# Kernel optimization log

Measured on AMD Instinct MI355X. Metric: run time of the kernel, lower is better.

Reference implementation:

```python
import jax, jax.numpy as jnp
import numpy as np

SEQ, B, N, F_IN = 128, 32, 1024, 16
NHID, G_FEAT, H = 2, 4, 256


def setup_inputs() -> dict:
    key = jax.random.key(0)
    ks = jax.random.split(key, 14)
    inp = {}
    inp['x'] = jax.random.normal(ks[0], (SEQ, B, N, F_IN), jnp.float32)
    # row-scaled random dense adjacency (keeps activations well-conditioned)
    inp['adj'] = jax.random.uniform(ks[1], (N, N), jnp.float32) * (1.0 / N)
    inp['gc1_w'] = jax.random.normal(ks[2], (F_IN, NHID), jnp.float32) * 0.3
    inp['gc1_b'] = jax.random.normal(ks[3], (NHID,), jnp.float32) * 0.1
    inp['gc2_w'] = jax.random.normal(ks[4], (NHID, G_FEAT), jnp.float32) * 0.3
    inp['gc2_b'] = jax.random.normal(ks[5], (G_FEAT,), jnp.float32) * 0.1
    in0 = G_FEAT * N  # GRU layer-0 input size = G_feat * num_nodes
    inp['w_ih_l0'] = jax.random.normal(ks[6], (3 * H, in0), jnp.float32) * 0.02
    inp['w_hh_l0'] = jax.random.normal(ks[7], (3 * H, H), jnp.float32) * 0.05
    inp['b_ih_l0'] = jax.random.normal(ks[8], (3 * H,), jnp.float32) * 0.05
    inp['b_hh_l0'] = jax.random.normal(ks[9], (3 * H,), jnp.float32) * 0.05
    inp['w_ih_l1'] = jax.random.normal(ks[10], (3 * H, H), jnp.float32) * 0.05
    inp['w_hh_l1'] = jax.random.normal(ks[11], (3 * H, H), jnp.float32) * 0.05
    inp['b_ih_l1'] = jax.random.normal(ks[12], (3 * H,), jnp.float32) * 0.05
    inp['b_hh_l1'] = jax.random.normal(ks[13], (3 * H,), jnp.float32) * 0.05
    return inp


def gru_layer(x_seq, h0, w_ih, w_hh, b_ih, b_hh):
    # torch nn.GRU gate math, gate order (r, z, n)
    def step(h, x_t):
        gi = x_t @ w_ih.T + b_ih          # (B, 3H)
        gh = h @ w_hh.T + b_hh            # (B, 3H)
        i_r, i_z, i_n = jnp.split(gi, 3, axis=-1)
        h_r, h_z, h_n = jnp.split(gh, 3, axis=-1)
        r = jax.nn.sigmoid(i_r + h_r)
        z = jax.nn.sigmoid(i_z + h_z)
        n = jnp.tanh(i_n + r * h_n)
        h_new = (1.0 - z) * n + z * h
        return h_new, h_new
    hT, out = jax.lax.scan(step, h0, x_seq)
    return out, hT


def reference(x, adj, gc1_w, gc1_b, gc2_w, gc2_b,
              w_ih_l0, w_hh_l0, b_ih_l0, b_hh_l0,
              w_ih_l1, w_hh_l1, b_ih_l1, b_hh_l1):
    # GCN, vectorized over (seq, batch). GraphConvolution: adj @ (x @ W) + b
    s = jnp.einsum('sbnf,fh->sbnh', x, gc1_w) + gc1_b
    s = jnp.einsum('mn,sbnh->sbmh', adj, s)
    s = jax.nn.relu(s)
    # dropout inactive in eval mode
    s = jnp.einsum('sbnh,hg->sbng', s, gc2_w) + gc2_b
    s = jnp.einsum('mn,sbng->sbmg', adj, s)
    s = jax.nn.log_softmax(s, axis=2)  # dim=1 of per-step (B, N, G) == node axis
    out = s.reshape(SEQ, B, N * G_FEAT)  # .view(batch, -1) per step, stacked
    h0 = jnp.zeros((B, H), out.dtype)
    out, h1 = gru_layer(out, h0, w_ih_l0, w_hh_l0, b_ih_l0, b_hh_l0)
    out, h2 = gru_layer(out, h0, w_ih_l1, w_hh_l1, b_ih_l1, b_hh_l1)
    hn = jnp.stack([h1, h2])  # (n_layers, B, H)
    return out, hn
```

## Files before the change

kernel.cpp:

```cpp
#include <hip/hip_runtime.h>
#include <stdint.h>

constexpr int SEQL = 128;
constexpr int BAT  = 32;
constexpr int NN   = 1024;
constexpr int FIN  = 16;
constexpr int HH   = 256;
constexpr int PQ   = SEQL * BAT;
constexpr float LSM_SHIFT = 6.9314718055994531f;

using f32x4 = __attribute__((ext_vector_type(4))) float;
using s16x8 = __attribute__((ext_vector_type(8))) short;

__device__ __forceinline__ unsigned short f2bf(float x) {
  unsigned u = __float_as_uint(x);
  u += 0x7fffu + ((u >> 16) & 1u);
  return (unsigned short)(u >> 16);
}
__device__ __forceinline__ float sigm(float x) { return 1.f / (1.f + __expf(-x)); }

__device__ __forceinline__ void gl_lds16(const void* g, void* l) {
  __builtin_amdgcn_global_load_lds(
      (const __attribute__((address_space(1))) void*)g,
      (__attribute__((address_space(3))) void*)l, 16, 0, 0);
}

#if __has_builtin(__builtin_amdgcn_fdot2_f32_bf16)
typedef __bf16 bf16x2_t __attribute__((ext_vector_type(2)));
__device__ __forceinline__ float dot2bf(unsigned w, unsigned h, float acc) {
  return __builtin_amdgcn_fdot2_f32_bf16(__builtin_bit_cast(bf16x2_t, w),
                                         __builtin_bit_cast(bf16x2_t, h), acc, false);
}
#else
__device__ __forceinline__ float dot2bf(unsigned w, unsigned h, float acc) {
  acc += __uint_as_float(w << 16) * __uint_as_float(h << 16);
  acc += __uint_as_float(w & 0xffff0000u) * __uint_as_float(h & 0xffff0000u);
  return acc;
}
#endif

__global__ __launch_bounds__(256) void k1_xw1(const float* __restrict__ x,
    const float* __restrict__ w1, const float* __restrict__ b1,
    unsigned short* __restrict__ Yt) {
  int idx = blockIdx.x * 256 + threadIdx.x;
  int p = idx >> 10, n = idx & 1023;
  const float* xp = x + (size_t)idx * FIN;
  float xv[16];
  *(float4*)(xv + 0)  = *(const float4*)(xp + 0);
  *(float4*)(xv + 4)  = *(const float4*)(xp + 4);
  *(float4*)(xv + 8)  = *(const float4*)(xp + 8);
  *(float4*)(xv + 12) = *(const float4*)(xp + 12);
  float y0 = b1[0], y1 = b1[1];
#pragma unroll
  for (int f = 0; f < 16; ++f) { y0 += xv[f] * w1[2*f]; y1 += xv[f] * w1[2*f+1]; }
  Yt[(size_t)(2*p)   * NN + n] = f2bf(y0);
  Yt[(size_t)(2*p+1) * NN + n] = f2bf(y1);
}

__global__ __launch_bounds__(256) void k_cvt(const float* __restrict__ in,
    unsigned short* __restrict__ out, int n4) {
  int i = blockIdx.x * 256 + threadIdx.x;
  if (i >= n4) return;
  float4 v = *(const float4*)(in + (size_t)i * 4);
  ushort4 o;
  o.x = f2bf(v.x); o.y = f2bf(v.y); o.z = f2bf(v.z); o.w = f2bf(v.w);
  *(ushort4*)(out + (size_t)i * 4) = o;
}

__global__ __launch_bounds__(256) void k_biasadj(const float* __restrict__ wih0,
    const float* __restrict__ bih0, float* __restrict__ biasAdj) {
  int wid = threadIdx.x >> 6, lane = threadIdx.x & 63;
  int j = blockIdx.x * 4 + wid;
  const float* row = wih0 + (size_t)j * 4096;
  float s = 0.f;
  for (int k = lane * 4; k < 4096; k += 256) {
    float4 v = *(const float4*)(row + k);
    s += v.x + v.y + v.z + v.w;
  }
#pragma unroll
  for (int off = 32; off >= 1; off >>= 1) s += __shfl_xor(s, off);
  if (lane == 0) biasAdj[j] = bih0[j] - LSM_SHIFT * s;
}

__global__ __launch_bounds__(256) void k_prep(const float* __restrict__ W,
    unsigned* __restrict__ Wp) {
  int tid = blockIdx.x * 256 + threadIdx.x;
  int j = tid >> 7, k2 = tid & 127;
  float2 wv = *(const float2*)(W + (size_t)j * 256 + 2 * k2);
  unsigned pk = (unsigned)f2bf(wv.x) | ((unsigned)f2bf(wv.y) << 16);
  int i = j >> 8, jg = j & 255, kg = k2 >> 6, c = (k2 >> 2) & 15, u = k2 & 3;
  Wp[(((i * 2 + kg) * 16 + c) << 10) + (jg << 2) + u] = pk;
}

template <int EPI>
__global__ __launch_bounds__(256) void gemm_bt(
    const unsigned short* __restrict__ A, const unsigned short* __restrict__ B,
    void* __restrict__ Cout, const float* __restrict__ bias, int K, int ldc) {
  __shared__ __align__(16) unsigned short As[128 * 64];
  __shared__ __align__(16) unsigned short Bs[128 * 64];
  const int tid = threadIdx.x;
  const int lane = tid & 63, wave = tid >> 6;
  const int ln15 = lane & 15, hi4 = lane >> 4;
  const int wr = wave >> 1, wc = wave & 1;
  const int m0 = blockIdx.y * 128, n0 = blockIdx.x * 128;
  const int rsub = lane >> 3, csub = lane & 7;

  f32x4 acc[4][4];
#pragma unroll
  for (int i = 0; i < 4; ++i)
#pragma unroll
    for (int j = 0; j < 4; ++j) acc[i][j] = {0.f, 0.f, 0.f, 0.f};

  for (int kt = 0; kt < K; kt += 64) {
    __syncthreads();
#pragma unroll
    for (int j = 0; j < 4; ++j) {
      int qq = wave * 4 + j;
      const unsigned short* ga = A + (size_t)(m0 + qq*8 + rsub) * K + kt + csub*8;
      gl_lds16(ga, &As[qq * 512]);
      const unsigned short* gb = B + (size_t)(n0 + qq*8 + rsub) * K + kt + csub*8;
      gl_lds16(gb, &Bs[qq * 512]);
    }
    __syncthreads();
#pragma unroll
    for (int kk = 0; kk < 2; ++kk) {
      s16x8 af[4], bfr[4];
#pragma unroll
      for (int mi = 0; mi < 4; ++mi)
        af[mi] = *(const s16x8*)&As[(wr*64 + mi*16 + ln15) * 64 + kk*32 + hi4*8];
#pragma unroll
      for (int ni = 0; ni < 4; ++ni)
        bfr[ni] = *(const s16x8*)&Bs[(wc*64 + ni*16 + ln15) * 64 + kk*32 + hi4*8];
#pragma unroll
      for (int mi = 0; mi < 4; ++mi)
#pragma unroll
        for (int ni = 0; ni < 4; ++ni)
          acc[mi][ni] = __builtin_amdgcn_mfma_f32_16x16x32_bf16(
              af[mi], bfr[ni], acc[mi][ni], 0, 0, 0);
    }
  }

  if (EPI == 2) {
    float* C = (float*)Cout;
#pragma unroll
    for (int ni = 0; ni < 4; ++ni) {
      int j = n0 + wc*64 + ni*16 + ln15;
      float bv = bias[j];
#pragma unroll
      for (int mi = 0; mi < 4; ++mi) {
        int m = m0 + wr*64 + mi*16 + hi4*4;
#pragma unroll
        for (int r = 0; r < 4; ++r) C[(size_t)(m + r) * ldc + j] = acc[mi][ni][r] + bv;
      }
    }
  } else {
    unsigned short* C = (unsigned short*)Cout;
#pragma unroll
    for (int ni = 0; ni < 4; ++ni) {
      int j = n0 + wc*64 + ni*16 + ln15;
#pragma unroll
      for (int mi = 0; mi < 4; ++mi) {
        int m = m0 + wr*64 + mi*16 + hi4*4;
        ushort4 v;
        float f0 = acc[mi][ni][0], f1 = acc[mi][ni][1], f2 = acc[mi][ni][2], f3 = acc[mi][ni][3];
        if (EPI == 0) { f0 = fmaxf(f0, 0.f); f1 = fmaxf(f1, 0.f); f2 = fmaxf(f2, 0.f); f3 = fmaxf(f3, 0.f); }
        v.x = f2bf(f0); v.y = f2bf(f1); v.z = f2bf(f2); v.w = f2bf(f3);
        *(ushort4*)&C[(size_t)j * ldc + m] = v;
      }
    }
  }
}

__device__ __forceinline__ unsigned k4_proc(unsigned a, unsigned b, float w0, float w1, float bb) {
  float a0 = __uint_as_float(a << 16), a1 = __uint_as_float(a & 0xffff0000u);
  float b0 = __uint_as_float(b << 16), b1 = __uint_as_float(b & 0xffff0000u);
  float y0 = a0 * w0 + b0 * w1 + bb;
  float y1 = a1 * w0 + b1 * w1 + bb;
  return (unsigned)f2bf(y0) | ((unsigned)f2bf(y1) << 16);
}

__global__ __launch_bounds__(256) void k4_w2(const unsigned short* __restrict__ z1t,
    const float* __restrict__ w2, const float* __restrict__ b2,
    unsigned short* __restrict__ Y2t) {
  int idx = blockIdx.x * 256 + threadIdx.x;
  int j4 = idx >> 7, mb = idx & 127;
  int p = j4 >> 2, g = j4 & 3;
  const unsigned short* r0 = z1t + (size_t)(p * 2) * NN + mb * 8;
  const unsigned short* r1 = r0 + NN;
  float w0 = w2[g], w1v = w2[4 + g], bb = b2[g];
  uint4 ua = *(const uint4*)r0;
  uint4 ub = *(const uint4*)r1;
  uint4 o;
  o.x = k4_proc(ua.x, ub.x, w0, w1v, bb);
  o.y = k4_proc(ua.y, ub.y, w0, w1v, bb);
  o.z = k4_proc(ua.z, ub.z, w0, w1v, bb);
  o.w = k4_proc(ua.w, ub.w, w0, w1v, bb);
  *(uint4*)(Y2t + (size_t)j4 * NN + mb * 8) = o;
}

__global__ __launch_bounds__(256) void k6_lsm(const unsigned short* __restrict__ z2t,
    unsigned short* __restrict__ Xg) {
  int wid = threadIdx.x >> 6, lane = threadIdx.x & 63;
  int r = blockIdx.x * 4 + wid;
  int p = r >> 2, g = r & 3;
  const unsigned short* row = z2t + (size_t)r * NN;
  uint4 u0 = *(const uint4*)(row + lane * 16);
  uint4 u1 = *(const uint4*)(row + lane * 16 + 8);
  unsigned uu[8] = {u0.x, u0.y, u0.z, u0.w, u1.x, u1.y, u1.z, u1.w};
  float v[16];
#pragma unroll
  for (int q = 0; q < 8; ++q) {
    v[2*q]   = __uint_as_float(uu[q] << 16);
    v[2*q+1] = __uint_as_float(uu[q] & 0xffff0000u);
  }
  float mx = v[0];
#pragma unroll
  for (int e = 1; e < 16; ++e) mx = fmaxf(mx, v[e]);
#pragma unroll
  for (int off = 32; off >= 1; off >>= 1) mx = fmaxf(mx, __shfl_xor(mx, off));
  float s = 0.f;
#pragma unroll
  for (int e = 0; e < 16; ++e) s += __expf(v[e] - mx);
#pragma unroll
  for (int off = 32; off >= 1; off >>= 1) s += __shfl_xor(s, off);
  float lse = __logf(s) + mx;
  unsigned short* xr = Xg + (size_t)p * 4096;
#pragma unroll
  for (int e = 0; e < 16; ++e) xr[(lane * 16 + e) * 4 + g] = f2bf(v[e] - lse + LSM_SHIFT);
}

template <int L>
__global__ __launch_bounds__(512, 2) void k_rnn(const float* __restrict__ gi,
    const unsigned* __restrict__ Wp, const float* __restrict__ bhh,
    unsigned short* __restrict__ hb_out, float* __restrict__ hf_out,
    float* __restrict__ hn_row) {
  const int b = blockIdx.x, tid = threadIdx.x;
  const int jg = tid & 255, kg = tid >> 8;
  __shared__ __align__(16) unsigned hpk[128];
  __shared__ float part[2][776];

  uint4 w[3][16];
#pragma unroll
  for (int i = 0; i < 3; ++i)
#pragma unroll
    for (int c = 0; c < 16; ++c)
      w[i][c] = *(const uint4*)(Wp + ((((i * 2 + kg) * 16 + c) << 10) + (jg << 2)));

  float hprev = 0.f;
  float br = 0.f, bz = 0.f, bn = 0.f;
  float g0 = 0.f, g1 = 0.f, g2 = 0.f;
  if (tid < 256) {
    br = bhh[jg]; bz = bhh[256 + jg]; bn = bhh[512 + jg];
    const float* gr = gi + (size_t)(0 * BAT + b) * 768;
    g0 = gr[jg]; g1 = gr[256 + jg]; g2 = gr[512 + jg];
  }
  if (tid < 128) hpk[tid] = 0u;
  __syncthreads();

  for (int t = 0; t < SEQL; ++t) {
    float p0 = 0.f, p1 = 0.f, p2 = 0.f;
    if (tid < 256) {
      int tt = t + 1 < SEQL ? t + 1 : SEQL - 1;
      const float* gr = gi + (size_t)(tt * BAT + b) * 768;
      p0 = gr[jg]; p1 = gr[256 + jg]; p2 = gr[512 + jg];
    }
    float a0 = 0.f, a1 = 0.f, a2 = 0.f;
#pragma unroll
    for (int c = 0; c < 16; ++c) {
      uint4 hk = *(const uint4*)&hpk[kg * 64 + c * 4];
      a0 = dot2bf(w[0][c].x, hk.x, a0); a0 = dot2bf(w[0][c].y, hk.y, a0);
      a0 = dot2bf(w[0][c].z, hk.z, a0); a0 = dot2bf(w[0][c].w, hk.w, a0);
      a1 = dot2bf(w[1][c].x, hk.x, a1); a1 = dot2bf(w[1][c].y, hk.y, a1);
      a1 = dot2bf(w[1][c].z, hk.z, a1); a1 = dot2bf(w[1][c].w, hk.w, a1);
      a2 = dot2bf(w[2][c].x, hk.x, a2); a2 = dot2bf(w[2][c].y, hk.y, a2);
      a2 = dot2bf(w[2][c].z, hk.z, a2); a2 = dot2bf(w[2][c].w, hk.w, a2);
    }
    part[kg][jg]       = a0;
    part[kg][256 + jg] = a1;
    part[kg][512 + jg] = a2;
    __syncthreads();
    if (tid < 256) {
      float ghr = part[0][jg]       + part[1][jg]       + br;
      float ghz = part[0][256 + jg] + part[1][256 + jg] + bz;
      float ghn = part[0][512 + jg] + part[1][512 + jg] + bn;
      float r = sigm(g0 + ghr);
      float z = sigm(g1 + ghz);
      float nn = tanhf(g2 + r * ghn);
      float hnew = (1.f - z) * nn + z * hprev;
      hprev = hnew;
      unsigned short hbb = f2bf(hnew);
      if (L == 0) hb_out[(size_t)(t * BAT + b) * 256 + jg] = hbb;
      else        hf_out[(size_t)(t * BAT + b) * 256 + jg] = hnew;
      unsigned lo = (unsigned)hbb;
      unsigned hi = (unsigned)__shfl_down((int)lo, 1);
      if (!(jg & 1)) hpk[jg >> 1] = lo | (hi << 16);
      if (t == SEQL - 1) hn_row[b * 256 + jg] = hnew;
    }
    g0 = p0; g1 = p1; g2 = p2;
    __syncthreads();
  }
}

extern "C" void kernel_launch(void* const* d_in, const int* in_sizes, int n_in,
                              void* d_out, int out_size, void* d_ws, size_t ws_size,
                              hipStream_t stream) {
  const float* x    = (const float*)d_in[0];
  const float* adj  = (const float*)d_in[1];
  const float* gc1w = (const float*)d_in[2];
  const float* gc1b = (const float*)d_in[3];
  const float* gc2w = (const float*)d_in[4];
  const float* gc2b = (const float*)d_in[5];
  const float* wih0 = (const float*)d_in[6];
  const float* whh0 = (const float*)d_in[7];
  const float* bih0 = (const float*)d_in[8];
  const float* bhh0 = (const float*)d_in[9];
  const float* wih1 = (const float*)d_in[10];
  const float* whh1 = (const float*)d_in[11];
  const float* bih1 = (const float*)d_in[12];
  const float* bhh1 = (const float*)d_in[13];

  char* ws = (char*)d_ws;
  const size_t MB = 1048576;
  unsigned short* adjb  = (unsigned short*)(ws + 0);
  unsigned short* Yt    = (unsigned short*)(ws + 2 * MB);
  unsigned short* z1t   = (unsigned short*)(ws + 18 * MB);
  unsigned short* Y2t   = (unsigned short*)(ws + 34 * MB);
  unsigned short* z2t   = (unsigned short*)(ws + 2 * MB);
  unsigned short* Xg    = (unsigned short*)(ws + 34 * MB);
  unsigned short* wih0b = (unsigned short*)(ws + 2 * MB);
  float* biasAdj        = (float*)(ws + 9 * MB);
  float* gi0            = (float*)(ws + 10 * MB);
  unsigned* Whh0p       = (unsigned*)(ws + 23 * MB);
  unsigned* Whh1p       = (unsigned*)(ws + 24 * MB);
  unsigned short* wih1b = (unsigned short*)(ws + 25 * MB);
  unsigned short* h0b   = (unsigned short*)(ws + 25 * MB + 512 * 1024);
  float* gi1            = (float*)(ws + 28 * MB);
  float* out = (float*)d_out;
  float* hn  = out + (size_t)SEQL * BAT * HH;

  k1_xw1<<<PQ * NN / 256, 256, 0, stream>>>(x, gc1w, gc1b, Yt);
  k_cvt<<<(NN * NN / 4 + 255) / 256, 256, 0, stream>>>(adj, adjb, NN * NN / 4);
  gemm_bt<0><<<dim3(64, 8), 256, 0, stream>>>(adjb, Yt, (void*)z1t, nullptr, 1024, 1024);
  k4_w2<<<16384 * 128 / 256, 256, 0, stream>>>(z1t, gc2w, gc2b, Y2t);
  gemm_bt<1><<<dim3(128, 8), 256, 0, stream>>>(adjb, Y2t, (void*)z2t, nullptr, 1024, 1024);
  k6_lsm<<<16384 / 4, 256, 0, stream>>>(z2t, Xg);
  k_biasadj<<<192, 256, 0, stream>>>(wih0, bih0, biasAdj);
  k_cvt<<<(768 * 4096 / 4 + 255) / 256, 256, 0, stream>>>(wih0, wih0b, 768 * 4096 / 4);
  gemm_bt<2><<<dim3(6, 32), 256, 0, stream>>>(Xg, wih0b, (void*)gi0, biasAdj, 4096, 768);
  k_prep<<<384, 256, 0, stream>>>(whh0, Whh0p);
  k_prep<<<384, 256, 0, stream>>>(whh1, Whh1p);
  k_cvt<<<(768 * 256 / 4 + 255) / 256, 256, 0, stream>>>(wih1, wih1b, 768 * 256 / 4);
  k_rnn<0><<<32, 512, 0, stream>>>(gi0, Whh0p, bhh0, h0b, nullptr, hn);
  gemm_bt<2><<<dim3(6, 32), 256, 0, stream>>>(h0b, wih1b, (void*)gi1, bih1, 256, 768);
  k_rnn<1><<<32, 512, 0, stream>>>(gi1, Whh1p, bhh1, nullptr, out, hn + BAT * HH);
}
```

Baseline: 659.7 us.

## Split GRU recurrent weights across registers, LDS, and streamed global loads

Stops holding all 48 uint4 recurrent-weight chunks per thread in registers. The recurrent kernel now keeps 18 chunks in VGPRs, stages 18 in shared memory, and streams the remaining 12 from global/L2 each timestep through a small software prefetch queue. The weight prep layout is reindexed to match this split, and launch bounds drop to one block per SM. The goal is to avoid register spilling from the oversized weight array, at the cost of extra LDS traffic and per-step global loads on the latency-bound sequential loop.

```diff
diff --git a/kernel.cpp b/kernel.cpp
--- a/kernel.cpp
+++ b/kernel.cpp
@@ -11,6 +11,7 @@
 
 using f32x4 = __attribute__((ext_vector_type(4))) float;
 using s16x8 = __attribute__((ext_vector_type(8))) short;
+using u32x4 = __attribute__((ext_vector_type(4))) unsigned int;
 
 __device__ __forceinline__ unsigned short f2bf(float x) {
   unsigned u = __float_as_uint(x);
@@ -82,14 +83,15 @@
   if (lane == 0) biasAdj[j] = bih0[j] - LSM_SHIFT * s;
 }
 
-__global__ __launch_bounds__(256) void k_prep(const float* __restrict__ W,
+__global__ __launch_bounds__(256) void k_prepH(const float* __restrict__ W,
     unsigned* __restrict__ Wp) {
   int tid = blockIdx.x * 256 + threadIdx.x;
   int j = tid >> 7, k2 = tid & 127;
   float2 wv = *(const float2*)(W + (size_t)j * 256 + 2 * k2);
   unsigned pk = (unsigned)f2bf(wv.x) | ((unsigned)f2bf(wv.y) << 16);
-  int i = j >> 8, jg = j & 255, kg = k2 >> 6, c = (k2 >> 2) & 15, u = k2 & 3;
-  Wp[(((i * 2 + kg) * 16 + c) << 10) + (jg << 2) + u] = pk;
+  int i = j >> 8, jg = j & 255, kg = k2 >> 6, r = k2 & 63, c = r >> 2, u = r & 3;
+  int q = i * 16 + c, tidT = kg * 256 + jg;
+  Wp[(((size_t)q * 512 + tidT) << 2) + u] = pk;
 }
 
 template <int EPI>
@@ -230,7 +232,7 @@
 }
 
 template <int L>
-__global__ __launch_bounds__(512, 2) void k_rnn(const float* __restrict__ gi,
+__global__ __launch_bounds__(512, 1) void k_rnnH(const float* __restrict__ gi,
     const unsigned* __restrict__ Wp, const float* __restrict__ bhh,
     unsigned short* __restrict__ hb_out, float* __restrict__ hf_out,
     float* __restrict__ hn_row) {
@@ -238,24 +240,35 @@
   const int jg = tid & 255, kg = tid >> 8;
   __shared__ __align__(16) unsigned hpk[128];
   __shared__ float part[2][776];
-
-  uint4 w[3][16];
-#pragma unroll
-  for (int i = 0; i < 3; ++i)
-#pragma unroll
-    for (int c = 0; c < 16; ++c)
-      w[i][c] = *(const uint4*)(Wp + ((((i * 2 + kg) * 16 + c) << 10) + (jg << 2)));
+  __shared__ __align__(16) unsigned wlds[18 * 512 * 4];
+
+  unsigned w[18][4];
+#pragma unroll
+  for (int q = 0; q < 18; ++q) {
+    u32x4 t = *(const u32x4*)(Wp + (((size_t)q * 512 + tid) << 2));
+    w[q][0] = t.x; w[q][1] = t.y; w[q][2] = t.z; w[q][3] = t.w;
+#pragma unroll
+    for (int u = 0; u < 4; ++u) asm volatile("" : "+v"(w[q][u]));
+  }
+#pragma unroll
+  for (int cl = 0; cl < 18; ++cl) {
+    u32x4 t = *(const u32x4*)(Wp + (((size_t)(18 + cl) * 512 + tid) << 2));
+    *(u32x4*)&wlds[((size_t)cl * 512 + tid) * 4] = t;
+  }
+  const unsigned* Wstr = Wp + ((size_t)36 * 512 << 2);
 
   float hprev = 0.f;
   float br = 0.f, bz = 0.f, bn = 0.f;
   float g0 = 0.f, g1 = 0.f, g2 = 0.f;
   if (tid < 256) {
     br = bhh[jg]; bz = bhh[256 + jg]; bn = bhh[512 + jg];
-    const float* gr = gi + (size_t)(0 * BAT + b) * 768;
+    const float* gr = gi + (size_t)b * 768;
     g0 = gr[jg]; g1 = gr[256 + jg]; g2 = gr[512 + jg];
   }
   if (tid < 128) hpk[tid] = 0u;
   __syncthreads();
+
+#define STRLD(s) (*(const u32x4*)(Wstr + (((size_t)(s) * 512 + tid) << 2)))
 
   for (int t = 0; t < SEQL; ++t) {
     float p0 = 0.f, p1 = 0.f, p2 = 0.f;
@@ -265,15 +278,30 @@
       p0 = gr[jg]; p1 = gr[256 + jg]; p2 = gr[512 + jg];
     }
     float a0 = 0.f, a1 = 0.f, a2 = 0.f;
+    u32x4 s_a = STRLD(0), s_b = STRLD(1), s_c = STRLD(2);
 #pragma unroll
     for (int c = 0; c < 16; ++c) {
-      uint4 hk = *(const uint4*)&hpk[kg * 64 + c * 4];
-      a0 = dot2bf(w[0][c].x, hk.x, a0); a0 = dot2bf(w[0][c].y, hk.y, a0);
-      a0 = dot2bf(w[0][c].z, hk.z, a0); a0 = dot2bf(w[0][c].w, hk.w, a0);
-      a1 = dot2bf(w[1][c].x, hk.x, a1); a1 = dot2bf(w[1][c].y, hk.y, a1);
-      a1 = dot2bf(w[1][c].z, hk.z, a1); a1 = dot2bf(w[1][c].w, hk.w, a1);
-      a2 = dot2bf(w[2][c].x, hk.x, a2); a2 = dot2bf(w[2][c].y, hk.y, a2);
-      a2 = dot2bf(w[2][c].z, hk.z, a2); a2 = dot2bf(w[2][c].w, hk.w, a2);
+      u32x4 hk = *(const u32x4*)&hpk[kg * 64 + c * 4];
+      a0 = dot2bf(w[c][0], hk.x, a0); a0 = dot2bf(w[c][1], hk.y, a0);
+      a0 = dot2bf(w[c][2], hk.z, a0); a0 = dot2bf(w[c][3], hk.w, a0);
+      if (c < 2) {
+        a1 = dot2bf(w[16 + c][0], hk.x, a1); a1 = dot2bf(w[16 + c][1], hk.y, a1);
+        a1 = dot2bf(w[16 + c][2], hk.z, a1); a1 = dot2bf(w[16 + c][3], hk.w, a1);
+      } else {
+        u32x4 lv = *(const u32x4*)&wlds[((size_t)(c - 2) * 512 + tid) * 4];
+        a1 = dot2bf(lv.x, hk.x, a1); a1 = dot2bf(lv.y, hk.y, a1);
+        a1 = dot2bf(lv.z, hk.z, a1); a1 = dot2bf(lv.w, hk.w, a1);
+      }
+      if (c < 4) {
+        u32x4 lv = *(const u32x4*)&wlds[((size_t)(14 + c) * 512 + tid) * 4];
+        a2 = dot2bf(lv.x, hk.x, a2); a2 = dot2bf(lv.y, hk.y, a2);
+        a2 = dot2bf(lv.z, hk.z, a2); a2 = dot2bf(lv.w, hk.w, a2);
+      } else {
+        a2 = dot2bf(s_a.x, hk.x, a2); a2 = dot2bf(s_a.y, hk.y, a2);
+        a2 = dot2bf(s_a.z, hk.z, a2); a2 = dot2bf(s_a.w, hk.w, a2);
+        s_a = s_b; s_b = s_c;
+        if (c <= 12) s_c = STRLD(c - 1);
+      }
     }
     part[kg][jg]       = a0;
     part[kg][256 + jg] = a1;
@@ -299,6 +327,7 @@
     g0 = p0; g1 = p1; g2 = p2;
     __syncthreads();
   }
+#undef STRLD
 }
 
 extern "C" void kernel_launch(void* const* d_in, const int* in_sizes, int n_in,
@@ -347,10 +376,10 @@
   k_biasadj<<<192, 256, 0, stream>>>(wih0, bih0, biasAdj);
   k_cvt<<<(768 * 4096 / 4 + 255) / 256, 256, 0, stream>>>(wih0, wih0b, 768 * 4096 / 4);
   gemm_bt<2><<<dim3(6, 32), 256, 0, stream>>>(Xg, wih0b, (void*)gi0, biasAdj, 4096, 768);
-  k_prep<<<384, 256, 0, stream>>>(whh0, Whh0p);
-  k_prep<<<384, 256, 0, stream>>>(whh1, Whh1p);
+  k_prepH<<<384, 256, 0, stream>>>(whh0, Whh0p);
+  k_prepH<<<384, 256, 0, stream>>>(whh1, Whh1p);
   k_cvt<<<(768 * 256 / 4 + 255) / 256, 256, 0, stream>>>(wih1, wih1b, 768 * 256 / 4);
-  k_rnn<0><<<32, 512, 0, stream>>>(gi0, Whh0p, bhh0, h0b, nullptr, hn);
+  k_rnnH<0><<<32, 512, 0, stream>>>(gi0, Whh0p, bhh0, h0b, nullptr, hn);
   gemm_bt<2><<<dim3(6, 32), 256, 0, stream>>>(h0b, wih1b, (void*)gi1, bih1, 256, 768);
-  k_rnn<1><<<32, 512, 0, stream>>>(gi1, Whh1p, bhh1, nullptr, out, hn + BAT * HH);
-}
+  k_rnnH<1><<<32, 512, 0, stream>>>(gi1, Whh1p, bhh1, nullptr, out, hn + BAT * HH);
+}
```

New measurement: 695.3 us. +5.4%, slower.
